# Optimization experiments

Hardware: AMD Instinct MI355X
Metric: run time of the kernel (lower is better)

Reference implementation:

```python
import jax, jax.numpy as jnp
import numpy as np

K = 3          # kernel_size
H_BW = 0.5     # bandwidth 'h' in forward_chop


def _extract_patches(img, k):
    # Equivalent to F.conv2d(img, one_hot_kernel, stride=1, padding=0):
    # out channel index = c*k*k + ki*k + kj
    B, C, H, W = img.shape
    Ho, Wo = H - k + 1, W - k + 1
    sl = [img[:, :, i:i + Ho, j:j + Wo] for i in range(k) for j in range(k)]
    p = jnp.stack(sl, axis=2)                 # [B, C, k*k, Ho, Wo]
    return p.reshape(B, C * k * k, Ho, Wo)


def _pixel_shuffle(x, r):
    # torch F.pixel_shuffle: channel c*r*r + r1*r + r2 -> spatial (h*r+r1, w*r+r2)
    B, C, H, W = x.shape
    Co = C // (r * r)
    x = x.reshape(B, Co, r, r, H, W)
    x = x.transpose(0, 1, 4, 2, 5, 3)
    return x.reshape(B, Co, H * r, W * r)


def _overlap_add(patch, H, W, k, n_colors):
    # img_sum: strided pixel_shuffle overlap-add with ones-count normalization
    B = patch.shape[0]
    out = jnp.zeros((B, n_colors, H, W), patch.dtype)
    wei = jnp.zeros((1, 1, H, W), patch.dtype)
    ones = jnp.ones((1, k * k, patch.shape[2], patch.shape[3]), patch.dtype)
    for i in range(k):
        for j in range(k):
            px = _pixel_shuffle(patch[:, :, i::k, j::k], k)
            out = out.at[:, :, i:i + px.shape[2], j:j + px.shape[3]].add(px)
            wx = _pixel_shuffle(ones[:, :, i::k, j::k], k)
            wei = wei.at[:, :, i:i + wx.shape[2], j:j + wx.shape[3]].add(wx)
    return out / wei


def setup_inputs() -> dict:
    key = jax.random.key(0)
    kx, ky = jax.random.split(key)
    x = jax.random.normal(kx, (1, 3, 128, 128), dtype=jnp.float32)
    y = jax.random.normal(ky, (1, 3, 128, 128), dtype=jnp.float32)
    return {"x": x, "y": y}


def reference(x, y):
    # NonLocalModule.forward with h*w < min_size -> forward_chop(x, y)
    k = K
    B, C, H, W = x.shape
    ip = _extract_patches(x, k)               # [B, d, Ho, Wo], d = C*k*k
    rp = _extract_patches(y, k)
    d = ip.shape[1]
    L = ip.shape[2] * ip.shape[3]
    X = ip.reshape(B, d, L)                   # input patches  [B, d, L]
    XT = X.transpose(0, 2, 1)                 # [B, L, d]
    R = rp.reshape(B, d, L).transpose(0, 2, 1)  # refer patches [B, L, d]
    XY = jnp.einsum('bld,bdm->blm', R, X)     # [B, L, L]
    XX = jnp.sum(R * R, axis=2, keepdims=True)   # [B, L, 1]
    YY = jnp.sum(X * X, axis=1, keepdims=True)   # [B, 1, L]
    att = jax.nn.softmax((2.0 * XY - XX - YY) / (H_BW * H_BW + 0.1), axis=-1)
    out = jnp.einsum('blm,bmd->bld', att, XT)    # [B, L, d]
    out = out.transpose(0, 2, 1).reshape(ip.shape)
    return _overlap_add(out, H, W, k, C)
```

## Files before the change

### kernel.cpp

```cpp
#include <hip/hip_runtime.h>

#define LQv  15876
#define LP   16384
#define LQP  16384
#define HOc  126
#define NCH  16
#define C2L  8.243971662222648f
#define IC2L 0.1213006672795172f
#define CKS  4.121985831111324f

typedef __attribute__((ext_vector_type(8))) short bf16x8;
typedef __attribute__((ext_vector_type(4))) float f32x4;

#define MFMA(a,b,c) __builtin_amdgcn_mfma_f32_16x16x32_bf16((a),(b),(c),0,0,0)
#define EXP2(x) __builtin_amdgcn_exp2f(x)

__device__ __forceinline__ unsigned short f2bf_rne(float f) {
    unsigned u = __float_as_uint(f);
    unsigned r = ((u >> 16) & 1u) + 0x7FFFu;
    return (unsigned short)((u + r) >> 16);
}
__device__ __forceinline__ float bf2f(unsigned short h) {
    return __uint_as_float(((unsigned)h) << 16);
}
__device__ __forceinline__ void split_bf(float v, unsigned short& hi, unsigned short& lo) {
    hi = f2bf_rne(v);
    lo = f2bf_rne(v - bf2f(hi));
}
__device__ __forceinline__ constexpr int doffc(int d) {
    return (d / 9) * 16384 + ((d % 9) / 3) * 128 + ((d % 9) % 3);
}

__global__ __launch_bounds__(256) void prep_kernel(
    const float* __restrict__ x, const float* __restrict__ y,
    unsigned short* __restrict__ khi, unsigned short* __restrict__ klo,
    unsigned short* __restrict__ qhi, unsigned short* __restrict__ qlo,
    unsigned short* __restrict__ vt)
{
    int gidx = blockIdx.x * 256 + threadIdx.x;
    int pair = gidx >> 1, half = gidx & 1;
    int l = pair & (LP - 1);
    int role = pair >> 14;
    bool real = l < LQv;
    int i = real ? (l / HOc) : 0, j = real ? (l - i * HOc) : 0;
    int base = i * 128 + j;

    if (role < 2) {
        const float* __restrict__ src = role ? y : x;
        float scale = role ? C2L : 1.f;
        __align__(16) unsigned short hh[16], ll[16];
        float ss = 0.f;
#pragma unroll
        for (int it = 0; it < 16; ++it) {
            int offL = doffc(it);
            int offH = (16 + it < 27) ? doffc(16 + it) : 0;
            int off  = half ? offH : offL;
            bool ok  = (it < 11) ? real : (real && !half);
            float v = src[base + off];
            v = ok ? v : 0.f;
            ss = fmaf(v, v, ss);
            split_bf(scale * v, hh[it], ll[it]);
        }
        float tot = ss + __shfl_xor(ss, 1);
        if (half) {
            if (role == 0) {
                float ckv = real ? (-tot * CKS) : -1e30f;
                split_bf(ckv * IC2L, hh[11], ll[11]);
                hh[12] = ll[12] = 0;
                hh[13] = 0x3F80; ll[13] = 0;
                hh[14] = ll[14] = 0; hh[15] = ll[15] = 0;
            } else {
                split_bf(C2L, hh[11], ll[11]);
                hh[12] = ll[12] = 0;
                split_bf(80.f - CKS * tot, hh[13], ll[13]);
                hh[14] = ll[14] = 0; hh[15] = ll[15] = 0;
            }
        }
        int d0 = half << 4;
        unsigned short* dh = (role ? qhi : khi) + (size_t)l * 32 + d0;
        unsigned short* dl = (role ? qlo : klo) + (size_t)l * 32 + d0;
        ((uint4*)dh)[0] = ((uint4*)hh)[0]; ((uint4*)dh)[1] = ((uint4*)hh)[1];
        ((uint4*)dl)[0] = ((uint4*)ll)[0]; ((uint4*)dl)[1] = ((uint4*)ll)[1];
    } else {
        int kap = l & 31;
        int cp = 8 * ((kap >> 2) & 3) + 4 * (kap >> 4) + (kap & 3);
        int lp = (l & ~31) | cp;
        unsigned short* vbase = vt + lp + (half ? 16 * LP : 0);
#pragma unroll
        for (int it = 0; it < 16; ++it) {
            int offL = doffc(it);
            int offH = (16 + it < 27) ? doffc(16 + it) : 0;
            int off  = half ? offH : offL;
            bool ok  = (it < 11) ? real : (real && !half);
            float xv = x[base + off];
            unsigned short v;
            if (it == 11)
                v = ok ? f2bf_rne(xv) : ((real && half) ? (unsigned short)0x3F80
                                                        : (unsigned short)0);
            else
                v = ok ? f2bf_rne(xv) : 0;
            vbase[it * LP] = v;
        }
    }
}

__device__ __forceinline__ void gload16(const unsigned short* g, unsigned short* l)
{
    __builtin_amdgcn_global_load_lds(
        (__attribute__((address_space(1))) void*)g,
        (__attribute__((address_space(3))) void*)l, 16, 0, 0);
}

#define SLANE8(lane) ((((lane) & ~3) | (((lane) & 3) ^ (((lane) >> 3) & 3))) * 8)
#define SCHUNK8(lane) ((((lane) & 3) ^ (((lane) >> 3) & 3)) * 8)

__global__ __launch_bounds__(256, 4) void attn_kernel(
    const unsigned short* __restrict__ khi, const unsigned short* __restrict__ klo,
    const unsigned short* __restrict__ qhi, const unsigned short* __restrict__ qlo,
    const unsigned short* __restrict__ vt,  unsigned int* __restrict__ opart)
{
    __shared__ __align__(16) unsigned short lds[2][6144];
    int lane = threadIdx.x & 63;
    int wave = threadIdx.x >> 6;
    int n = lane & 15, g = lane >> 4;
    int gx = g ^ ((n >> 1) & 3);
    int qb = blockIdx.x * 256 + wave * 64;
    int ch = blockIdx.y;

    bf16x8 bqh[4], bql[4];
#pragma unroll
    for (int t = 0; t < 4; ++t) {
        bqh[t] = *(const bf16x8*)(qhi + (size_t)(qb + t * 16 + n) * 32 + g * 8);
        bql[t] = *(const bf16x8*)(qlo + (size_t)(qb + t * 16 + n) * 32 + g * 8);
    }

    f32x4 o0[4], o1[4];
#pragma unroll
    for (int t = 0; t < 4; ++t) {
        o0[t] = (f32x4){0.f, 0.f, 0.f, 0.f};
        o1[t] = (f32x4){0.f, 0.f, 0.f, 0.f};
    }

    int kb0 = ch * 1024;

#define STAGE(dst, kb) do {                                                   \
        if (wave == 0) {                                                      \
            gload16(khi + (size_t)(kb) * 32 +        SLANE8(lane), (dst));    \
            gload16(khi + (size_t)(kb) * 32 +  512 + SLANE8(lane), (dst) + 512);\
            gload16(khi + (size_t)(kb) * 32 + 1024 + SLANE8(lane), (dst) + 1024);\
            gload16(khi + (size_t)(kb) * 32 + 1536 + SLANE8(lane), (dst) + 1536);\
        } else if (wave == 1) {                                               \
            gload16(klo + (size_t)(kb) * 32 +        SLANE8(lane), (dst) + 2048);\
            gload16(klo + (size_t)(kb) * 32 +  512 + SLANE8(lane), (dst) + 2560);\
            gload16(klo + (size_t)(kb) * 32 + 1024 + SLANE8(lane), (dst) + 3072);\
            gload16(klo + (size_t)(kb) * 32 + 1536 + SLANE8(lane), (dst) + 3584);\
        } else if (wave == 2) {                                               \
            gload16(vt + (size_t)(lane >> 2) * LP + (kb) + SCHUNK8(lane),     \
                    (dst) + 4096);                                            \
            gload16(vt + (size_t)(16 + (lane >> 2)) * LP + (kb) + SCHUNK8(lane), \
                    (dst) + 4608);                                            \
        } else {                                                              \
            gload16(vt + (size_t)(lane >> 2) * LP + (kb) + 32 + SCHUNK8(lane),\
                    (dst) + 5120);                                            \
            gload16(vt + (size_t)(16 + (lane >> 2)) * LP + (kb) + 32 + SCHUNK8(lane), \
                    (dst) + 5632);                                            \
        }                                                                     \
    } while (0)

    STAGE(lds[0], kb0);
    __syncthreads();

    int buf = 0;
    for (int it = 0; it < 16; ++it) {
        int kbn = kb0 + ((it + 1) & 15) * 64;
        STAGE(lds[buf ^ 1], kbn);
        __builtin_amdgcn_sched_barrier(0);

        const unsigned short* L = lds[buf];
#pragma unroll
        for (int h = 0; h < 2; ++h) {
            bf16x8 kh0 = *(const bf16x8*)(L + (32 * h + n) * 32 + gx * 8);
            bf16x8 kh1 = *(const bf16x8*)(L + (32 * h + 16 + n) * 32 + gx * 8);
            bf16x8 kl0 = *(const bf16x8*)(L + 2048 + (32 * h + n) * 32 + gx * 8);
            bf16x8 kl1 = *(const bf16x8*)(L + 2048 + (32 * h + 16 + n) * 32 + gx * 8);
            bf16x8 v0  = *(const bf16x8*)(L + 4096 + h * 1024 + n * 32 + gx * 8);
            bf16x8 v1  = *(const bf16x8*)(L + 4096 + h * 1024 + (16 + n) * 32 + gx * 8);

#pragma unroll
            for (int qt = 0; qt < 4; ++qt) {
                f32x4 cc0 = {0.f, 0.f, 0.f, 0.f}, cc1 = {0.f, 0.f, 0.f, 0.f};
                cc0 = MFMA(kh0, bqh[qt], cc0); cc1 = MFMA(kh1, bqh[qt], cc1);
                cc0 = MFMA(kh0, bql[qt], cc0); cc1 = MFMA(kh1, bql[qt], cc1);
                cc0 = MFMA(kl0, bqh[qt], cc0); cc1 = MFMA(kl1, bqh[qt], cc1);
                float p0 = EXP2(cc0[0]);
                float p1 = EXP2(cc0[1]);
                float p2 = EXP2(cc0[2]);
                float p3 = EXP2(cc0[3]);
                float p4 = EXP2(cc1[0]);
                float p5 = EXP2(cc1[1]);
                float p6 = EXP2(cc1[2]);
                float p7 = EXP2(cc1[3]);
                union { unsigned u[4]; bf16x8 v; } ap;
                ap.u[0] = __builtin_amdgcn_perm(__float_as_uint(p1), __float_as_uint(p0), 0x07060302u);
                ap.u[1] = __builtin_amdgcn_perm(__float_as_uint(p3), __float_as_uint(p2), 0x07060302u);
                ap.u[2] = __builtin_amdgcn_perm(__float_as_uint(p5), __float_as_uint(p4), 0x07060302u);
                ap.u[3] = __builtin_amdgcn_perm(__float_as_uint(p7), __float_as_uint(p6), 0x07060302u);
                o0[qt] = MFMA(ap.v, v0, o0[qt]);
                o1[qt] = MFMA(ap.v, v1, o1[qt]);
            }
        }
        __syncthreads();
        buf ^= 1;
    }
#undef STAGE

#pragma unroll
    for (int qt = 0; qt < 4; ++qt) {
#pragma unroll
        for (int r = 0; r < 4; ++r) {
            unsigned w = ((unsigned)f2bf_rne(o1[qt][r]) << 16) | f2bf_rne(o0[qt][r]);
            size_t row = (size_t)ch * LQP + qb + qt * 16 + 4 * g + r;
            opart[row * 16 + n] = w;
        }
    }
}

__global__ __launch_bounds__(256) void final_kernel(
    const unsigned int* __restrict__ opart, float* __restrict__ out)
{
    __shared__ float lpatch[100 * 32];
    int tid = threadIdx.x;
    int lane = tid & 63;
    int h0 = (blockIdx.x >> 4) * 8, w0 = (blockIdx.x & 15) * 8;

    for (int t = tid; t < 1600; t += 256) {
        int rr = t >> 4, n = t & 15;
        int di = rr / 10, dj = rr - di * 10;
        int I = h0 - 2 + di, J = w0 - 2 + dj;
        bool valid = ((unsigned)I < 126u) && ((unsigned)J < 126u);
        int l = valid ? (I * HOc + J) : 0;
        float s0 = 0.f, s1 = 0.f;
#pragma unroll
        for (int c = 0; c < NCH; ++c) {
            unsigned v = opart[((size_t)c * LQP + l) * 16 + n];
            s0 += bf2f((unsigned short)(v & 0xffffu));
            s1 += bf2f((unsigned short)(v >> 16));
        }
        float denom = __shfl(s1, (lane & 48) | 11);
        float inv = 1.f / denom;
        lpatch[rr * 32 + n]      = s0 * inv;
        lpatch[rr * 32 + 16 + n] = s1 * inv;
    }
    __syncthreads();

    if (tid < 192) {
        int c = tid >> 6, pix = tid & 63;
        int h = h0 + (pix >> 3), w = w0 + (pix & 7);
        float sum = 0.f; int cnt = 0;
#pragma unroll
        for (int r1 = 0; r1 < 3; ++r1) {
            int I = h - r1; if ((unsigned)I >= 126u) continue;
#pragma unroll
            for (int r2 = 0; r2 < 3; ++r2) {
                int J = w - r2; if ((unsigned)J >= 126u) continue;
                int rr = (I - (h0 - 2)) * 10 + (J - (w0 - 2));
                sum += lpatch[rr * 32 + c * 9 + r1 * 3 + r2];
                ++cnt;
            }
        }
        out[c * 16384 + h * 128 + w] = sum / (float)cnt;
    }
}

extern "C" void kernel_launch(void* const* d_in, const int* in_sizes, int n_in,
                              void* d_out, int out_size, void* d_ws, size_t ws_size,
                              hipStream_t stream)
{
    const float* x = (const float*)d_in[0];
    const float* y = (const float*)d_in[1];
    float* out = (float*)d_out;

    unsigned short* khi = (unsigned short*)d_ws;
    unsigned short* klo = khi + (size_t)LP * 32;
    unsigned short* qhi = klo + (size_t)LP * 32;
    unsigned short* qlo = qhi + (size_t)LQP * 32;
    unsigned short* vt  = qlo + (size_t)LQP * 32;
    unsigned int* opart = (unsigned int*)(vt + (size_t)32 * LP);

    dim3 blk(256);
    prep_kernel <<<dim3(384),     blk, 0, stream>>>(x, y, khi, klo, qhi, qlo, vt);
    attn_kernel <<<dim3(64, NCH), blk, 0, stream>>>(khi, klo, qhi, qlo, vt, opart);
    final_kernel<<<dim3(256),     blk, 0, stream>>>(opart, out);
}
```

Baseline: 120.8 us.

## Fuse prep, attention and final kernels into one persistent kernel with grid barriers

Merges the three launches into a single kernel of 512 blocks. Blocks hand off between phases through atomic grid barriers, whose counters live in the first words of the output buffer and are zeroed by a memset. Each attention block now covers two key chunks in sequence instead of one, halving the attention grid. The goal is to remove launch gaps between the stages. In exchange, per-CU occupancy during attention drops, and the barrier only works if all 512 blocks are resident at the same time.

New measurement: 276.2 us. 129% more time.

```diff
diff --git a/kernel.cpp b/kernel.cpp
--- a/kernel.cpp
+++ b/kernel.cpp
@@ -31,13 +31,30 @@
     return (d / 9) * 16384 + ((d % 9) / 3) * 128 + ((d % 9) % 3);
 }
 
-__global__ __launch_bounds__(256) void prep_kernel(
+
+__device__ __forceinline__ void bar_arrive(unsigned* c) {
+    __syncthreads();
+    if (threadIdx.x == 0) {
+        __threadfence();
+        __hip_atomic_fetch_add(c, 1u, __ATOMIC_RELEASE, __HIP_MEMORY_SCOPE_AGENT);
+    }
+}
+__device__ __forceinline__ void bar_wait(unsigned* c, unsigned n) {
+    if (threadIdx.x == 0) {
+        while (__hip_atomic_load(c, __ATOMIC_ACQUIRE, __HIP_MEMORY_SCOPE_AGENT) < n)
+            __builtin_amdgcn_s_sleep(8);
+        __threadfence();
+    }
+    __syncthreads();
+}
+
+__device__ __forceinline__ void prep_phase(int bid, int tid,
     const float* __restrict__ x, const float* __restrict__ y,
     unsigned short* __restrict__ khi, unsigned short* __restrict__ klo,
     unsigned short* __restrict__ qhi, unsigned short* __restrict__ qlo,
     unsigned short* __restrict__ vt)
 {
-    int gidx = blockIdx.x * 256 + threadIdx.x;
+    int gidx = bid * 256 + tid;
     int pair = gidx >> 1, half = gidx & 1;
     int l = pair & (LP - 1);
     int role = pair >> 14;
@@ -110,22 +127,20 @@
         (__attribute__((address_space(1))) void*)g,
         (__attribute__((address_space(3))) void*)l, 16, 0, 0);
 }
-
 #define SLANE8(lane) ((((lane) & ~3) | (((lane) & 3) ^ (((lane) >> 3) & 3))) * 8)
 #define SCHUNK8(lane) ((((lane) & 3) ^ (((lane) >> 3) & 3)) * 8)
 
-__global__ __launch_bounds__(256, 4) void attn_kernel(
+__device__ __forceinline__ void attn_phase(int bid, int tid, unsigned short* lds,
     const unsigned short* __restrict__ khi, const unsigned short* __restrict__ klo,
     const unsigned short* __restrict__ qhi, const unsigned short* __restrict__ qlo,
     const unsigned short* __restrict__ vt,  unsigned int* __restrict__ opart)
 {
-    __shared__ __align__(16) unsigned short lds[2][6144];
-    int lane = threadIdx.x & 63;
-    int wave = threadIdx.x >> 6;
+    int lane = tid & 63;
+    int wave = tid >> 6;
     int n = lane & 15, g = lane >> 4;
     int gx = g ^ ((n >> 1) & 3);
-    int qb = blockIdx.x * 256 + wave * 64;
-    int ch = blockIdx.y;
+    int qbx = bid & 63, chp = bid >> 6;
+    int qb = qbx * 256 + wave * 64;
 
     bf16x8 bqh[4], bql[4];
 #pragma unroll
@@ -134,14 +149,8 @@
         bql[t] = *(const bf16x8*)(qlo + (size_t)(qb + t * 16 + n) * 32 + g * 8);
     }
 
-    f32x4 o0[4], o1[4];
-#pragma unroll
-    for (int t = 0; t < 4; ++t) {
-        o0[t] = (f32x4){0.f, 0.f, 0.f, 0.f};
-        o1[t] = (f32x4){0.f, 0.f, 0.f, 0.f};
-    }
-
-    int kb0 = ch * 1024;
+    unsigned short* B0 = lds;
+    unsigned short* B1 = lds + 6144;
 
 #define STAGE(dst, kb) do {                                                   \
         if (wave == 0) {                                                      \
@@ -167,71 +176,82 @@
         }                                                                     \
     } while (0)
 
-    STAGE(lds[0], kb0);
-    __syncthreads();
-
-    int buf = 0;
-    for (int it = 0; it < 16; ++it) {
-        int kbn = kb0 + ((it + 1) & 15) * 64;
-        STAGE(lds[buf ^ 1], kbn);
-        __builtin_amdgcn_sched_barrier(0);
-
-        const unsigned short* L = lds[buf];
-#pragma unroll
-        for (int h = 0; h < 2; ++h) {
-            bf16x8 kh0 = *(const bf16x8*)(L + (32 * h + n) * 32 + gx * 8);
-            bf16x8 kh1 = *(const bf16x8*)(L + (32 * h + 16 + n) * 32 + gx * 8);
-            bf16x8 kl0 = *(const bf16x8*)(L + 2048 + (32 * h + n) * 32 + gx * 8);
-            bf16x8 kl1 = *(const bf16x8*)(L + 2048 + (32 * h + 16 + n) * 32 + gx * 8);
-            bf16x8 v0  = *(const bf16x8*)(L + 4096 + h * 1024 + n * 32 + gx * 8);
-            bf16x8 v1  = *(const bf16x8*)(L + 4096 + h * 1024 + (16 + n) * 32 + gx * 8);
-
-#pragma unroll
-            for (int qt = 0; qt < 4; ++qt) {
-                f32x4 cc0 = {0.f, 0.f, 0.f, 0.f}, cc1 = {0.f, 0.f, 0.f, 0.f};
-                cc0 = MFMA(kh0, bqh[qt], cc0); cc1 = MFMA(kh1, bqh[qt], cc1);
-                cc0 = MFMA(kh0, bql[qt], cc0); cc1 = MFMA(kh1, bql[qt], cc1);
-                cc0 = MFMA(kl0, bqh[qt], cc0); cc1 = MFMA(kl1, bqh[qt], cc1);
-                float p0 = EXP2(cc0[0]);
-                float p1 = EXP2(cc0[1]);
-                float p2 = EXP2(cc0[2]);
-                float p3 = EXP2(cc0[3]);
-                float p4 = EXP2(cc1[0]);
-                float p5 = EXP2(cc1[1]);
-                float p6 = EXP2(cc1[2]);
-                float p7 = EXP2(cc1[3]);
-                union { unsigned u[4]; bf16x8 v; } ap;
-                ap.u[0] = __builtin_amdgcn_perm(__float_as_uint(p1), __float_as_uint(p0), 0x07060302u);
-                ap.u[1] = __builtin_amdgcn_perm(__float_as_uint(p3), __float_as_uint(p2), 0x07060302u);
-                ap.u[2] = __builtin_amdgcn_perm(__float_as_uint(p5), __float_as_uint(p4), 0x07060302u);
-                ap.u[3] = __builtin_amdgcn_perm(__float_as_uint(p7), __float_as_uint(p6), 0x07060302u);
-                o0[qt] = MFMA(ap.v, v0, o0[qt]);
-                o1[qt] = MFMA(ap.v, v1, o1[qt]);
+    for (int cc = 0; cc < 2; ++cc) {
+        int ch = chp + cc * 8;
+        int kb0 = ch * 1024;
+
+        f32x4 o0[4], o1[4];
+#pragma unroll
+        for (int t = 0; t < 4; ++t) {
+            o0[t] = (f32x4){0.f, 0.f, 0.f, 0.f};
+            o1[t] = (f32x4){0.f, 0.f, 0.f, 0.f};
+        }
+
+        STAGE(B0, kb0);
+        __syncthreads();
+
+        for (int it = 0; it < 16; ++it) {
+            int kbn = kb0 + ((it + 1) & 15) * 64;
+            unsigned short* cur = (it & 1) ? B1 : B0;
+            unsigned short* nxt = (it & 1) ? B0 : B1;
+            STAGE(nxt, kbn);
+            __builtin_amdgcn_sched_barrier(0);
+
+            const unsigned short* L = cur;
+#pragma unroll
+            for (int h = 0; h < 2; ++h) {
+                bf16x8 kh0 = *(const bf16x8*)(L + (32 * h + n) * 32 + gx * 8);
+                bf16x8 kh1 = *(const bf16x8*)(L + (32 * h + 16 + n) * 32 + gx * 8);
+                bf16x8 kl0 = *(const bf16x8*)(L + 2048 + (32 * h + n) * 32 + gx * 8);
+                bf16x8 kl1 = *(const bf16x8*)(L + 2048 + (32 * h + 16 + n) * 32 + gx * 8);
+                bf16x8 v0  = *(const bf16x8*)(L + 4096 + h * 1024 + n * 32 + gx * 8);
+                bf16x8 v1  = *(const bf16x8*)(L + 4096 + h * 1024 + (16 + n) * 32 + gx * 8);
+
+#pragma unroll
+                for (int qt = 0; qt < 4; ++qt) {
+                    f32x4 cc0 = {0.f, 0.f, 0.f, 0.f}, cc1 = {0.f, 0.f, 0.f, 0.f};
+                    cc0 = MFMA(kh0, bqh[qt], cc0); cc1 = MFMA(kh1, bqh[qt], cc1);
+                    cc0 = MFMA(kh0, bql[qt], cc0); cc1 = MFMA(kh1, bql[qt], cc1);
+                    cc0 = MFMA(kl0, bqh[qt], cc0); cc1 = MFMA(kl1, bqh[qt], cc1);
+                    float p0 = EXP2(cc0[0]);
+                    float p1 = EXP2(cc0[1]);
+                    float p2 = EXP2(cc0[2]);
+                    float p3 = EXP2(cc0[3]);
+                    float p4 = EXP2(cc1[0]);
+                    float p5 = EXP2(cc1[1]);
+                    float p6 = EXP2(cc1[2]);
+                    float p7 = EXP2(cc1[3]);
+                    union { unsigned u[4]; bf16x8 v; } ap;
+                    ap.u[0] = __builtin_amdgcn_perm(__float_as_uint(p1), __float_as_uint(p0), 0x07060302u);
+                    ap.u[1] = __builtin_amdgcn_perm(__float_as_uint(p3), __float_as_uint(p2), 0x07060302u);
+                    ap.u[2] = __builtin_amdgcn_perm(__float_as_uint(p5), __float_as_uint(p4), 0x07060302u);
+                    ap.u[3] = __builtin_amdgcn_perm(__float_as_uint(p7), __float_as_uint(p6), 0x07060302u);
+                    o0[qt] = MFMA(ap.v, v0, o0[qt]);
+                    o1[qt] = MFMA(ap.v, v1, o1[qt]);
+                }
             }
+            __syncthreads();
+        }
+
+#pragma unroll
+        for (int qt = 0; qt < 4; ++qt) {
+#pragma unroll
+            for (int r = 0; r < 4; ++r) {
+                unsigned w = ((unsigned)f2bf_rne(o1[qt][r]) << 16) | f2bf_rne(o0[qt][r]);
+                size_t row = (size_t)ch * LQP + qb + qt * 16 + 4 * g + r;
+                opart[row * 16 + n] = w;
+            }
         }
         __syncthreads();
-        buf ^= 1;
     }
 #undef STAGE
-
-#pragma unroll
-    for (int qt = 0; qt < 4; ++qt) {
-#pragma unroll
-        for (int r = 0; r < 4; ++r) {
-            unsigned w = ((unsigned)f2bf_rne(o1[qt][r]) << 16) | f2bf_rne(o0[qt][r]);
-            size_t row = (size_t)ch * LQP + qb + qt * 16 + 4 * g + r;
-            opart[row * 16 + n] = w;
-        }
-    }
-}
-
-__global__ __launch_bounds__(256) void final_kernel(
+}
+
+__device__ __forceinline__ void final_phase(int bid, int tid, float* lpatch,
     const unsigned int* __restrict__ opart, float* __restrict__ out)
 {
-    __shared__ float lpatch[100 * 32];
-    int tid = threadIdx.x;
     int lane = tid & 63;
-    int h0 = (blockIdx.x >> 4) * 8, w0 = (blockIdx.x & 15) * 8;
+    int h0 = (bid >> 4) * 8, w0 = (bid & 15) * 8;
 
     for (int t = tid; t < 1600; t += 256) {
         int rr = t >> 4, n = t & 15;
@@ -272,6 +292,32 @@
     }
 }
 
+__global__ __launch_bounds__(256, 4) void fused_kernel(
+    const float* __restrict__ x, const float* __restrict__ y,
+    unsigned short* __restrict__ khi, unsigned short* __restrict__ klo,
+    unsigned short* __restrict__ qhi, unsigned short* __restrict__ qlo,
+    unsigned short* __restrict__ vt,  unsigned int* __restrict__ opart,
+    float* __restrict__ out)
+{
+    __shared__ __align__(16) unsigned short smem[2][6144];
+    int bid = blockIdx.x, tid = threadIdx.x;
+    unsigned* barA = (unsigned*)out;
+    unsigned* barB = (unsigned*)out + 1;
+
+    if (bid < 384)
+        prep_phase(bid, tid, x, y, khi, klo, qhi, qlo, vt);
+    bar_arrive(barA);
+    bar_wait(barA, 512);
+
+    attn_phase(bid, tid, &smem[0][0], khi, klo, qhi, qlo, vt, opart);
+    bar_arrive(barB);
+
+    if (bid < 256) {
+        bar_wait(barB, 512);
+        final_phase(bid, tid, (float*)&smem[0][0], opart, out);
+    }
+}
+
 extern "C" void kernel_launch(void* const* d_in, const int* in_sizes, int n_in,
                               void* d_out, int out_size, void* d_ws, size_t ws_size,
                               hipStream_t stream)
@@ -287,8 +333,8 @@
     unsigned short* vt  = qlo + (size_t)LQP * 32;
     unsigned int* opart = (unsigned int*)(vt + (size_t)32 * LP);
 
-    dim3 blk(256);
-    prep_kernel <<<dim3(384),     blk, 0, stream>>>(x, y, khi, klo, qhi, qlo, vt);
-    attn_kernel <<<dim3(64, NCH), blk, 0, stream>>>(khi, klo, qhi, qlo, vt, opart);
-    final_kernel<<<dim3(256),     blk, 0, stream>>>(opart, out);
-}
+    hipMemsetAsync(out, 0, 2 * sizeof(unsigned), stream);
+
+    fused_kernel<<<dim3(512), dim3(256), 0, stream>>>(
+        x, y, khi, klo, qhi, qlo, vt, opart, out);
+}
```
